# Optimization experiments

Measured on AMD Instinct MI355X. Metric: run time of the kernel, lower is better.

## Reference

```python
import jax, jax.numpy as jnp
import numpy as np

B, S, D = 4, 4096, 1024
GATE_THR = 0.0
ADAPT_RATIO = 0.25
MIN_K = 1
Q_MIX = 0.5
Q_WIN = 3
Q_THR = 0.5
Q_TEMP = 0.1
BUDGET_K = 2048  # ceil(0.5 * S)
CB_MIX = 0.3
CB_SIZE = 16
CB_TEMP = 0.1
CB_TOPK = 4


def setup_inputs() -> dict:
    key = jax.random.key(0)
    ks = jax.random.split(key, 6)
    x = jax.random.normal(ks[0], (B, S, D), dtype=jnp.float32)
    Wq = jax.random.normal(ks[1], (D, D), dtype=jnp.float32) * 0.02
    Wk = jax.random.normal(ks[2], (D, D), dtype=jnp.float32) * 0.02
    Wg = jax.random.normal(ks[3], (D, D), dtype=jnp.float32) * 0.02
    bg = jnp.zeros((D,), dtype=jnp.float32)
    Wm = jax.random.normal(ks[4], (D, D), dtype=jnp.float32) * 0.02
    bm = jnp.zeros((D,), dtype=jnp.float32)
    Wc = jax.random.normal(ks[5], (CB_SIZE, D), dtype=jnp.float32) * 0.02
    return {"x": x, "Wq": Wq, "Wk": Wk, "Wg": Wg, "bg": bg, "Wm": Wm, "bm": bm, "Wc": Wc}


def reference(x, Wq, Wk, Wg, bg, Wm, bm, Wc):
    # --- symplectic twist: cross-product area of consecutive (q, k) transitions ---
    q = x @ Wq.T                                 # [B,S,D]
    k = x @ Wk.T                                 # [B,S,D]
    twist = q[:, :-1] * k[:, 1:] - q[:, 1:] * k[:, :-1]   # [B,S-1,D]
    twist = jnp.pad(twist, ((0, 0), (1, 0), (0, 0)))       # pad first step -> [B,S,D]

    # --- gated SAE-style projection with adaptive top-k sparsity mask ---
    gate_pre = x @ Wg.T + bg                     # [B,S,D]
    strength = jnp.tanh(jnp.mean(jnp.abs(gate_pre), axis=-1, keepdims=True))
    kk = jnp.clip(jnp.ceil(strength * (ADAPT_RATIO * D)).astype(jnp.int32), MIN_K, D)  # [B,S,1]
    order = jnp.argsort(-gate_pre, axis=-1)      # descending rank order
    ranks = jnp.argsort(order, axis=-1)          # inverse permutation: rank of each feature
    topk_mask = ranks < kk                       # keep top-k features per token
    gate = ((gate_pre > GATE_THR) & topk_mask).astype(x.dtype)  # hard gate
    mag = jax.nn.relu(x @ Wm.T + bm)
    mu = gate * mag * twist                      # gated moment-map features [B,S,D]

    complexity = jnp.mean(jnp.abs(mu), axis=-1, keepdims=True)  # [B,S,1]

    # --- quorum consensus smoothing (avg_pool1d, count_include_pad) + budgeted top-k ---
    pad = Q_WIN // 2
    cpad = jnp.pad(complexity, ((0, 0), (pad, pad), (0, 0)))
    cs = jnp.pad(jnp.cumsum(cpad, axis=1), ((0, 0), (1, 0), (0, 0)))
    local = (cs[:, Q_WIN:] - cs[:, :-Q_WIN]) / Q_WIN            # [B,S,1] sliding mean
    quorum = jax.nn.sigmoid((local - Q_THR) / Q_TEMP)
    qr = quorum[..., 0]                                          # [B,S]
    top_idx = jax.lax.top_k(qr, BUDGET_K)[1]                     # [B,BUDGET_K]
    bmask = jnp.zeros_like(qr, dtype=bool).at[jnp.arange(B)[:, None], top_idx].set(True)
    quorum = jnp.where(bmask[..., None], quorum, 0.0)
    complexity = complexity * (1.0 - Q_MIX + Q_MIX * quorum)

    # --- codebook soft-assignment + top-k renorm + temporal shift score ---
    logits = (x @ Wc.T) / CB_TEMP                                # [B,S,CB_SIZE]
    probs = jax.nn.softmax(logits, axis=-1)
    ti = jax.lax.top_k(probs, CB_TOPK)[1]                        # [B,S,CB_TOPK]
    cmask = jnp.zeros(probs.shape, dtype=bool).at[
        jnp.arange(B)[:, None, None], jnp.arange(S)[None, :, None], ti].set(True)
    probs = jnp.where(cmask, probs, 0.0)
    probs = probs / jnp.clip(jnp.sum(probs, axis=-1, keepdims=True), 1e-8)
    shift = 0.5 * jnp.sum(jnp.abs(probs[:, 1:] - probs[:, :-1]), axis=-1, keepdims=True)
    cb_score = jnp.pad(shift, ((0, 0), (1, 0), (0, 0)))          # [B,S,1]

    complexity = (1.0 - CB_MIX) * complexity + CB_MIX * cb_score
    return complexity
```

## Files before the change

### kernel.cpp

```cpp
#include <hip/hip_runtime.h>
#include <hip/hip_bf16.h>
#include <cstdint>

#define BB 4
#define SS 4096
#define DD 1024
#define MM (BB * SS)
#define NTOT 4096
#define BUDGET 2048

typedef __attribute__((ext_vector_type(8))) short short8v;
typedef __attribute__((ext_vector_type(4))) float f32x4;

__device__ __forceinline__ float bf2f(unsigned int h) {
  return __uint_as_float(h << 16);
}
__device__ __forceinline__ unsigned short f2bf(float f) {
  unsigned int u = __float_as_uint(f);
  u = u + 0x7FFFu + ((u >> 16) & 1u);
  return (unsigned short)(u >> 16);
}
__device__ __forceinline__ unsigned int pkbf(float lo, float hi) {
  float2 f; f.x = lo; f.y = hi;
  __hip_bfloat162 h = __float22bfloat162_rn(f);
  return *(unsigned int*)&h;
}

__global__ __launch_bounds__(256) void convert2_kernel(
    const float* __restrict__ x,
    const float* __restrict__ Wq, const float* __restrict__ Wk,
    const float* __restrict__ Wg, const float* __restrict__ Wm,
    const float* __restrict__ Wc,
    unsigned short* __restrict__ xb, unsigned short* __restrict__ Wb,
    float* __restrict__ probs)
{
  const int blk = blockIdx.x;
  const int t = threadIdx.x;
  if (blk < 4096) {
    const int wv = t >> 6, ln = t & 63;
    const int token = blk * 4 + wv;
    const size_t rowo = (size_t)token * DD;
    const float4* x4 = (const float4*)(x + rowo);
    const float4* Wc4 = (const float4*)Wc;
    float4 xv[4];
    #pragma unroll
    for (int e = 0; e < 4; ++e) xv[e] = x4[e * 64 + ln];
    uint2* xo = (uint2*)(xb + rowo);
    #pragma unroll
    for (int e = 0; e < 4; ++e) {
      uint2 o; o.x = pkbf(xv[e].x, xv[e].y); o.y = pkbf(xv[e].z, xv[e].w);
      xo[e * 64 + ln] = o;
    }
    float pj[16];
    #pragma unroll
    for (int j = 0; j < 16; ++j) {
      float a = 0.f;
      #pragma unroll
      for (int e = 0; e < 4; ++e) {
        const float4 w = Wc4[j * 256 + e * 64 + ln];
        a += xv[e].x * w.x + xv[e].y * w.y + xv[e].z * w.z + xv[e].w * w.w;
      }
      pj[j] = a;
    }
    #pragma unroll
    for (int j = 0; j < 16; ++j) {
      #pragma unroll
      for (int off = 1; off < 64; off <<= 1) pj[j] += __shfl_xor(pj[j], off);
    }
    if (ln == 0) {
      float p[16];
      float mx = -3.4e38f;
      #pragma unroll
      for (int j = 0; j < 16; ++j) { p[j] = pj[j] * 10.0f; mx = fmaxf(mx, p[j]); }
      float se = 0.f;
      #pragma unroll
      for (int j = 0; j < 16; ++j) { p[j] = expf(p[j] - mx); se += p[j]; }
      const float inv = 1.0f / se;
      #pragma unroll
      for (int j = 0; j < 16; ++j) p[j] *= inv;
      unsigned int mk = 0;
      for (int it = 0; it < 4; ++it) {
        int bi = 0; float bv = -1.f;
        #pragma unroll
        for (int j = 0; j < 16; ++j)
          if (!((mk >> j) & 1u) && p[j] > bv) { bv = p[j]; bi = j; }
        mk |= 1u << bi;
      }
      float ssum = 0.f;
      #pragma unroll
      for (int j = 0; j < 16; ++j) if ((mk >> j) & 1u) ssum += p[j];
      const float rinv = 1.0f / fmaxf(ssum, 1e-8f);
      #pragma unroll
      for (int j = 0; j < 16; ++j)
        probs[(size_t)token * 16 + j] = ((mk >> j) & 1u) ? p[j] * rinv : 0.f;
    }
  } else {
    const size_t off0 = (size_t)(blk - 4096) * 2048 + t * 8;
    const int m = (int)(off0 >> 20);
    const float* Ws = (m == 0) ? Wq : (m == 1) ? Wk : (m == 2) ? Wg : Wm;
    const size_t wo = off0 & 1048575u;
    const float4 a0 = *(const float4*)(Ws + wo);
    const float4 a1 = *(const float4*)(Ws + wo + 4);
    uint4 o;
    o.x = pkbf(a0.x, a0.y); o.y = pkbf(a0.z, a0.w);
    o.z = pkbf(a1.x, a1.y); o.w = pkbf(a1.z, a1.w);
    *(uint4*)(Wb + off0) = o;
  }
}

__global__ __launch_bounds__(1024, 4) void gemm256_kernel(
    const unsigned short* __restrict__ xb, const unsigned short* __restrict__ Wb,
    const float* __restrict__ bg, const float* __restrict__ bm,
    unsigned short* __restrict__ qb, unsigned short* __restrict__ kb,
    unsigned short* __restrict__ gb, unsigned short* __restrict__ mb)
{
  __shared__ __align__(16) unsigned short lds[32768];
  const int t  = threadIdx.x;
  const int wv = t >> 6, ln = t & 63;
  const int wr = wv >> 2, wc = wv & 3;
  const int frow = ln & 15, kc = ln >> 4;

  const int o  = blockIdx.y * 16 + blockIdx.x;
  const int L  = (o & 7) * 128 + (o >> 3);
  const int bx = L & 15, by = L >> 4;
  const int m0 = by * 256;
  const int n0 = bx * 256;
  const int mat = n0 >> 10;
  const int nc0 = n0 & 1023;

  f32x4 acc[4][4];
  #pragma unroll
  for (int i = 0; i < 4; ++i)
    #pragma unroll
    for (int j = 0; j < 4; ++j) { acc[i][j][0]=0.f; acc[i][j][1]=0.f; acc[i][j][2]=0.f; acc[i][j][3]=0.f; }

  const int grow = t >> 2;
  const int gch  = (((t & 3) ^ ((t >> 2) & 3)) << 3);
  auto stage = [&](int buf, int kt) {
    const int k0 = kt << 5;
    const unsigned short* ga = xb + (size_t)(m0 + grow) * DD + k0 + gch;
    const unsigned short* gw = Wb + (size_t)(n0 + grow) * DD + k0 + gch;
    __builtin_amdgcn_global_load_lds(
        (const __attribute__((address_space(1))) void*)ga,
        (__attribute__((address_space(3))) void*)((__attribute__((address_space(3))) char*)lds
            + buf * 32768 + t * 16),
        16, 0, 0);
    __builtin_amdgcn_global_load_lds(
        (const __attribute__((address_space(1))) void*)gw,
        (__attribute__((address_space(3))) void*)((__attribute__((address_space(3))) char*)lds
            + buf * 32768 + 16384 + t * 16),
        16, 0, 0);
  };

  stage(0, 0);
  const int sl = ((kc ^ (frow & 3)) << 3);

  for (int kt = 0; kt < 32; ++kt) {
    const int cur = kt & 1;
    if (kt < 31) {
      stage(cur ^ 1, kt + 1);
      asm volatile("s_waitcnt vmcnt(2)" ::: "memory");
    } else {
      asm volatile("s_waitcnt vmcnt(0)" ::: "memory");
    }
    __builtin_amdgcn_s_barrier();
    asm volatile("" ::: "memory");

    short8v a[4], b[4];
    #pragma unroll
    for (int i = 0; i < 4; ++i)
      a[i] = *(const short8v*)&lds[cur * 16384 + (wr * 64 + i * 16 + frow) * 32 + sl];
    #pragma unroll
    for (int j = 0; j < 4; ++j)
      b[j] = *(const short8v*)&lds[cur * 16384 + 8192 + (wc * 64 + j * 16 + frow) * 32 + sl];

    #pragma unroll
    for (int i = 0; i < 4; ++i)
      #pragma unroll
      for (int j = 0; j < 4; ++j)
        acc[i][j] = __builtin_amdgcn_mfma_f32_16x16x32_bf16(a[i], b[j], acc[i][j], 0, 0, 0);

    asm volatile("" ::: "memory");
    __builtin_amdgcn_s_barrier();
  }

  unsigned short* outp = (mat == 0) ? qb : (mat == 1) ? kb : (mat == 2) ? gb : mb;
  #pragma unroll
  for (int i = 0; i < 4; ++i) {
    #pragma unroll
    for (int j = 0; j < 4; ++j) {
      const int col = nc0 + wc * 64 + j * 16 + frow;
      const float bias = (mat == 2) ? bg[col] : (mat == 3) ? bm[col] : 0.f;
      #pragma unroll
      for (int r = 0; r < 4; ++r) {
        const int row = m0 + wr * 64 + i * 16 + kc * 4 + r;
        float v = acc[i][j][r] + bias;
        if (mat == 3) v = fmaxf(v, 0.0f);
        outp[(size_t)row * DD + col] = f2bf(v);
      }
    }
  }
}

__global__ __launch_bounds__(256) void mfma_gemm_fb(
    const float* __restrict__ x,
    const float* __restrict__ Wq, const float* __restrict__ Wk,
    const float* __restrict__ Wg, const float* __restrict__ Wm,
    const float* __restrict__ bg, const float* __restrict__ bm,
    unsigned short* __restrict__ q_o, unsigned short* __restrict__ k_o,
    unsigned short* __restrict__ g_o, unsigned short* __restrict__ m_o)
{
  __shared__ __align__(16) unsigned short As[128 * 32];
  __shared__ __align__(16) unsigned short Bs[128 * 32];
  const int t  = threadIdx.x;
  const int wv = t >> 6, ln = t & 63;
  const int wr = wv >> 1, wc = wv & 1;
  const int m0 = blockIdx.y * 128;
  const int n0 = blockIdx.x * 128;
  const int mat = n0 >> 10;
  const int nc0 = n0 & 1023;
  const float* __restrict__ Wsrc = (mat == 0) ? Wq : (mat == 1) ? Wk : (mat == 2) ? Wg : Wm;

  f32x4 acc[4][4];
  #pragma unroll
  for (int i = 0; i < 4; ++i)
    #pragma unroll
    for (int j = 0; j < 4; ++j) { acc[i][j][0]=0.f; acc[i][j][1]=0.f; acc[i][j][2]=0.f; acc[i][j][3]=0.f; }

  const int frow = ln & 15, kc = ln >> 4;

  for (int k0 = 0; k0 < DD; k0 += 32) {
    #pragma unroll
    for (int c = 0; c < 2; ++c) {
      const int i = c * 256 + t;
      const int row = i >> 2, colc = i & 3;
      const float* ga = x    + (size_t)(m0 + row) * DD + k0 + (colc << 3);
      const float* gw = Wsrc + (size_t)(nc0 + row) * DD + k0 + (colc << 3);
      const float4 a0 = *(const float4*)ga, a1 = *(const float4*)(ga + 4);
      const float4 b0 = *(const float4*)gw, b1 = *(const float4*)(gw + 4);
      uint4 ao, bo;
      ao.x = pkbf(a0.x, a0.y); ao.y = pkbf(a0.z, a0.w);
      ao.z = pkbf(a1.x, a1.y); ao.w = pkbf(a1.z, a1.w);
      bo.x = pkbf(b0.x, b0.y); bo.y = pkbf(b0.z, b0.w);
      bo.z = pkbf(b1.x, b1.y); bo.w = pkbf(b1.z, b1.w);
      *(uint4*)&As[row * 32 + colc * 8] = ao;
      *(uint4*)&Bs[row * 32 + colc * 8] = bo;
    }
    __syncthreads();
    short8v a[4], b[4];
    #pragma unroll
    for (int i = 0; i < 4; ++i) {
      a[i] = *(const short8v*)&As[(wr * 64 + i * 16 + frow) * 32 + kc * 8];
      b[i] = *(const short8v*)&Bs[(wc * 64 + i * 16 + frow) * 32 + kc * 8];
    }
    #pragma unroll
    for (int i = 0; i < 4; ++i)
      #pragma unroll
      for (int j = 0; j < 4; ++j)
        acc[i][j] = __builtin_amdgcn_mfma_f32_16x16x32_bf16(a[i], b[j], acc[i][j], 0, 0, 0);
    __syncthreads();
  }

  unsigned short* outp = (mat == 0) ? q_o : (mat == 1) ? k_o : (mat == 2) ? g_o : m_o;
  #pragma unroll
  for (int i = 0; i < 4; ++i) {
    #pragma unroll
    for (int j = 0; j < 4; ++j) {
      const int col = nc0 + wc * 64 + j * 16 + frow;
      #pragma unroll
      for (int r = 0; r < 4; ++r) {
        const int row = m0 + wr * 64 + i * 16 + kc * 4 + r;
        float v = acc[i][j][r];
        if (mat == 2) v += bg[col];
        if (mat == 3) v = fmaxf(v + bm[col], 0.0f);
        outp[(size_t)row * DD + col] = f2bf(v);
      }
    }
  }
}

__global__ __launch_bounds__(256) void token_kernel3(
    const unsigned short* __restrict__ qb, const unsigned short* __restrict__ kb,
    const unsigned short* __restrict__ gb, const unsigned short* __restrict__ mb,
    float* __restrict__ craw)
{
  const int wv = threadIdx.x >> 6;
  const int ln = threadIdx.x & 63;
  const int token = blockIdx.x * 4 + wv;
  const int s = token & (SS - 1);
  const size_t rowo = (size_t)token * DD;

  if (s == 0) { if (ln == 0) craw[token] = 0.f; return; }

  unsigned short gbit[16];
  *(uint4*)&gbit[0] = *(const uint4*)(gb + rowo + ln * 16);
  *(uint4*)&gbit[8] = *(const uint4*)(gb + rowo + ln * 16 + 8);
  int ckey[16];
  float asum = 0.f;
  #pragma unroll
  for (int i = 0; i < 16; ++i) {
    const unsigned int b = gbit[i];
    ckey[i] = (b & 0x8000u) ? (int)(b ^ 0xFFFFu) : (int)(b | 0x8000u);
    asum += bf2f(b & 0x7FFFu);
  }
  #pragma unroll
  for (int off = 1; off < 64; off <<= 1) asum += __shfl_xor(asum, off);
  const float strength = tanhf(asum * (1.0f / 1024.0f));
  int kkv = (int)ceilf(strength * 256.0f);
  kkv = min(max(kkv, 1), 1024);

  int lo = 0, hi = 0xFFFF;
  while (lo < hi) {
    const int mid = (lo + hi + 1) >> 1;
    int c = 0;
    #pragma unroll
    for (int i = 0; i < 16; ++i) c += (ckey[i] >= mid);
    #pragma unroll
    for (int off = 1; off < 64; off <<= 1) c += __shfl_xor(c, off);
    if (c >= kkv) lo = mid; else hi = mid - 1;
  }
  const int T = lo;

  int cg = 0, myeq = 0;
  #pragma unroll
  for (int i = 0; i < 16; ++i) { cg += (ckey[i] > T); myeq += (ckey[i] == T); }
  #pragma unroll
  for (int off = 1; off < 64; off <<= 1) cg += __shfl_xor(cg, off);
  int incl = myeq;
  #pragma unroll
  for (int off = 1; off < 64; off <<= 1) {
    const int tt = __shfl_up(incl, off);
    if (ln >= off) incl += tt;
  }
  int ebase = incl - myeq;
  const int keep_eq = kkv - cg;

  unsigned short mB[16], qcB[16], kcB[16], qpB[16], kpB[16];
  *(uint4*)&mB[0]  = *(const uint4*)(mb + rowo + ln * 16);
  *(uint4*)&mB[8]  = *(const uint4*)(mb + rowo + ln * 16 + 8);
  *(uint4*)&qcB[0] = *(const uint4*)(qb + rowo + ln * 16);
  *(uint4*)&qcB[8] = *(const uint4*)(qb + rowo + ln * 16 + 8);
  *(uint4*)&kcB[0] = *(const uint4*)(kb + rowo + ln * 16);
  *(uint4*)&kcB[8] = *(const uint4*)(kb + rowo + ln * 16 + 8);
  *(uint4*)&qpB[0] = *(const uint4*)(qb + rowo - DD + ln * 16);
  *(uint4*)&qpB[8] = *(const uint4*)(qb + rowo - DD + ln * 16 + 8);
  *(uint4*)&kpB[0] = *(const uint4*)(kb + rowo - DD + ln * 16);
  *(uint4*)&kpB[8] = *(const uint4*)(kb + rowo - DD + ln * 16 + 8);

  float accv = 0.f;
  #pragma unroll
  for (int i = 0; i < 16; ++i) {
    const bool kp_ = (ckey[i] > T) || (ckey[i] == T && ebase < keep_eq);
    if (ckey[i] == T) ebase++;
    const unsigned int b = gbit[i];
    const bool gpos = (!(b & 0x8000u)) && (b != 0u);
    if (gpos && kp_) {
      const float tw = bf2f(qpB[i]) * bf2f(kcB[i]) - bf2f(qcB[i]) * bf2f(kpB[i]);
      accv += bf2f(mB[i]) * fabsf(tw);
    }
  }
  #pragma unroll
  for (int off = 1; off < 64; off <<= 1) accv += __shfl_xor(accv, off);
  if (ln == 0) craw[token] = accv * (1.0f / 1024.0f);
}

__global__ __launch_bounds__(256) void token_kernel2(
    const float* __restrict__ x, const float* __restrict__ Wc,
    const unsigned short* __restrict__ qb, const unsigned short* __restrict__ kb,
    const unsigned short* __restrict__ gb, const unsigned short* __restrict__ mb,
    float* __restrict__ probs, float* __restrict__ craw)
{
  const int wv = threadIdx.x >> 6;
  const int ln = threadIdx.x & 63;
  const int token = blockIdx.x * 4 + wv;
  const int s = token & (SS - 1);
  const size_t rowo = (size_t)token * DD;

  const float4* x4 = (const float4*)(x + rowo);
  const float4* Wc4 = (const float4*)Wc;
  float4 xv[4];
  #pragma unroll
  for (int e = 0; e < 4; ++e) xv[e] = x4[e * 64 + ln];
  float pj[16];
  #pragma unroll
  for (int j = 0; j < 16; ++j) {
    float a = 0.f;
    #pragma unroll
    for (int e = 0; e < 4; ++e) {
      const float4 w = Wc4[j * 256 + e * 64 + ln];
      a += xv[e].x * w.x + xv[e].y * w.y + xv[e].z * w.z + xv[e].w * w.w;
    }
    pj[j] = a;
  }
  #pragma unroll
  for (int j = 0; j < 16; ++j) {
    #pragma unroll
    for (int off = 1; off < 64; off <<= 1) pj[j] += __shfl_xor(pj[j], off);
  }
  if (ln == 0) {
    float p[16];
    float mx = -3.4e38f;
    #pragma unroll
    for (int j = 0; j < 16; ++j) { p[j] = pj[j] * 10.0f; mx = fmaxf(mx, p[j]); }
    float se = 0.f;
    #pragma unroll
    for (int j = 0; j < 16; ++j) { p[j] = expf(p[j] - mx); se += p[j]; }
    const float inv = 1.0f / se;
    #pragma unroll
    for (int j = 0; j < 16; ++j) p[j] *= inv;
    unsigned int mk = 0;
    for (int it = 0; it < 4; ++it) {
      int bi = 0; float bv = -1.f;
      #pragma unroll
      for (int j = 0; j < 16; ++j)
        if (!((mk >> j) & 1u) && p[j] > bv) { bv = p[j]; bi = j; }
      mk |= 1u << bi;
    }
    float ssum = 0.f;
    #pragma unroll
    for (int j = 0; j < 16; ++j) if ((mk >> j) & 1u) ssum += p[j];
    const float rinv = 1.0f / fmaxf(ssum, 1e-8f);
    #pragma unroll
    for (int j = 0; j < 16; ++j)
      probs[(size_t)token * 16 + j] = ((mk >> j) & 1u) ? p[j] * rinv : 0.f;
  }

  if (s == 0) { if (ln == 0) craw[token] = 0.f; return; }

  unsigned short gbit[16];
  *(uint4*)&gbit[0] = *(const uint4*)(gb + rowo + ln * 16);
  *(uint4*)&gbit[8] = *(const uint4*)(gb + rowo + ln * 16 + 8);
  int ckey[16];
  float asum = 0.f;
  #pragma unroll
  for (int i = 0; i < 16; ++i) {
    const unsigned int b = gbit[i];
    ckey[i] = (b & 0x8000u) ? (int)(b ^ 0xFFFFu) : (int)(b | 0x8000u);
    asum += bf2f(b & 0x7FFFu);
  }
  #pragma unroll
  for (int off = 1; off < 64; off <<= 1) asum += __shfl_xor(asum, off);
  const float strength = tanhf(asum * (1.0f / 1024.0f));
  int kkv = (int)ceilf(strength * 256.0f);
  kkv = min(max(kkv, 1), 1024);

  int lo = 0, hi = 0xFFFF;
  while (lo < hi) {
    const int mid = (lo + hi + 1) >> 1;
    int c = 0;
    #pragma unroll
    for (int i = 0; i < 16; ++i) c += (ckey[i] >= mid);
    #pragma unroll
    for (int off = 1; off < 64; off <<= 1) c += __shfl_xor(c, off);
    if (c >= kkv) lo = mid; else hi = mid - 1;
  }
  const int T = lo;

  int cg = 0, myeq = 0;
  #pragma unroll
  for (int i = 0; i < 16; ++i) { cg += (ckey[i] > T); myeq += (ckey[i] == T); }
  #pragma unroll
  for (int off = 1; off < 64; off <<= 1) cg += __shfl_xor(cg, off);
  int incl = myeq;
  #pragma unroll
  for (int off = 1; off < 64; off <<= 1) {
    const int tt = __shfl_up(incl, off);
    if (ln >= off) incl += tt;
  }
  int ebase = incl - myeq;
  const int keep_eq = kkv - cg;

  unsigned short mB[16], qcB[16], kcB[16], qpB[16], kpB[16];
  *(uint4*)&mB[0]  = *(const uint4*)(mb + rowo + ln * 16);
  *(uint4*)&mB[8]  = *(const uint4*)(mb + rowo + ln * 16 + 8);
  *(uint4*)&qcB[0] = *(const uint4*)(qb + rowo + ln * 16);
  *(uint4*)&qcB[8] = *(const uint4*)(qb + rowo + ln * 16 + 8);
  *(uint4*)&kcB[0] = *(const uint4*)(kb + rowo + ln * 16);
  *(uint4*)&kcB[8] = *(const uint4*)(kb + rowo + ln * 16 + 8);
  *(uint4*)&qpB[0] = *(const uint4*)(qb + rowo - DD + ln * 16);
  *(uint4*)&qpB[8] = *(const uint4*)(qb + rowo - DD + ln * 16 + 8);
  *(uint4*)&kpB[0] = *(const uint4*)(kb + rowo - DD + ln * 16);
  *(uint4*)&kpB[8] = *(const uint4*)(kb + rowo - DD + ln * 16 + 8);

  float accv = 0.f;
  #pragma unroll
  for (int i = 0; i < 16; ++i) {
    const bool kp_ = (ckey[i] > T) || (ckey[i] == T && ebase < keep_eq);
    if (ckey[i] == T) ebase++;
    const unsigned int b = gbit[i];
    const bool gpos = (!(b & 0x8000u)) && (b != 0u);
    if (gpos && kp_) {
      const float tw = bf2f(qpB[i]) * bf2f(kcB[i]) - bf2f(qcB[i]) * bf2f(kpB[i]);
      accv += bf2f(mB[i]) * fabsf(tw);
    }
  }
  #pragma unroll
  for (int off = 1; off < 64; off <<= 1) accv += __shfl_xor(accv, off);
  if (ln == 0) craw[token] = accv * (1.0f / 1024.0f);
}

__global__ __launch_bounds__(256) void quorum_kernel(
    const float* __restrict__ craw, const float* __restrict__ probs,
    float* __restrict__ quorum, float* __restrict__ cb)
{
  const int idx = blockIdx.x * 256 + threadIdx.x;
  const int s = idx & (SS - 1);
  const float c1 = craw[idx];
  const float c0 = (s > 0) ? craw[idx - 1] : 0.f;
  const float c2 = (s < SS - 1) ? craw[idx + 1] : 0.f;
  const float local = (c0 + c1 + c2) / 3.0f;
  quorum[idx] = 1.0f / (1.0f + expf((0.5f - local) * 10.0f));
  float sh = 0.f;
  if (s > 0) {
    #pragma unroll
    for (int j = 0; j < 16; ++j)
      sh += fabsf(probs[(size_t)idx * 16 + j] - probs[(size_t)(idx - 1) * 16 + j]);
  }
  cb[idx] = 0.5f * sh;
}

__global__ __launch_bounds__(64) void final_kernel(
    const float* __restrict__ craw, const float* __restrict__ quorum,
    const float* __restrict__ cb, float* __restrict__ outp)
{
  const int b = blockIdx.x;
  const int ln = threadIdx.x;
  const size_t base = (size_t)b * SS;
  float qv[64]; unsigned int key[64];
  #pragma unroll
  for (int i = 0; i < 64; ++i) {
    qv[i] = quorum[base + ln * 64 + i];
    const unsigned int bb = __float_as_uint(qv[i]);
    key[i] = (bb & 0x80000000u) ? ~bb : (bb | 0x80000000u);
  }
  unsigned int lo = 0u, hi = 0xFFFFFFFFu;
  while (lo < hi) {
    const unsigned int mid = (unsigned int)(((unsigned long long)lo + hi + 1ull) >> 1);
    int c = 0;
    #pragma unroll
    for (int i = 0; i < 64; ++i) c += (key[i] >= mid);
    #pragma unroll
    for (int off = 1; off < 64; off <<= 1) c += __shfl_xor(c, off);
    if (c >= BUDGET) lo = mid; else hi = mid - 1;
  }
  const unsigned int T = lo;
  int cg = 0, myeq = 0;
  #pragma unroll
  for (int i = 0; i < 64; ++i) { cg += (key[i] > T); myeq += (key[i] == T); }
  #pragma unroll
  for (int off = 1; off < 64; off <<= 1) cg += __shfl_xor(cg, off);
  int scan = myeq;
  #pragma unroll
  for (int off = 1; off < 64; off <<= 1) {
    const int nsc = __shfl_up(scan, off);
    if (ln >= off) scan += nsc;
  }
  int ebase = scan - myeq;
  const int keep_eq = BUDGET - cg;
  #pragma unroll
  for (int i = 0; i < 64; ++i) {
    const size_t sidx = base + (size_t)ln * 64 + i;
    const bool kp_ = (key[i] > T) || (key[i] == T && ebase < keep_eq);
    if (key[i] == T) ebase++;
    const float q = kp_ ? qv[i] : 0.f;
    outp[sidx] = 0.7f * (craw[sidx] * (0.5f + 0.5f * q)) + 0.3f * cb[sidx];
  }
}

extern "C" void kernel_launch(void* const* d_in, const int* in_sizes, int n_in,
                              void* d_out, int out_size, void* d_ws, size_t ws_size,
                              hipStream_t stream)
{
  const float* x  = (const float*)d_in[0];
  const float* Wq = (const float*)d_in[1];
  const float* Wk = (const float*)d_in[2];
  const float* Wg = (const float*)d_in[3];
  const float* bg = (const float*)d_in[4];
  const float* Wm = (const float*)d_in[5];
  const float* bm = (const float*)d_in[6];
  const float* Wc = (const float*)d_in[7];
  float* outp = (float*)d_out;
  char* w = (char*)d_ws;

  const size_t SZ_BF = (size_t)MM * DD * 2;
  const size_t SMALL_OFF = 4 * SZ_BF;
  const size_t SZ_SMALL = 1048576 + 3 * 65536;

  unsigned short* qb = (unsigned short*)(w);
  unsigned short* kb = (unsigned short*)(w + SZ_BF);
  unsigned short* gb = (unsigned short*)(w + 2 * SZ_BF);
  unsigned short* mb = (unsigned short*)(w + 3 * SZ_BF);
  char* sm = w + SMALL_OFF;
  float* probs  = (float*)(sm);
  float* craw   = (float*)(sm + 1048576);
  float* quorum = (float*)(sm + 1048576 + 65536);
  float* cbuf   = (float*)(sm + 1048576 + 2 * 65536);

  const size_t need_mid = SMALL_OFF + SZ_SMALL + SZ_BF + (size_t)4 * 1048576 * 2;

  if (ws_size >= need_mid) {
    unsigned short* xb = (unsigned short*)(sm + SZ_SMALL);
    unsigned short* Wb = xb + (size_t)MM * DD;
    convert2_kernel<<<dim3(4096 + 2048), 256, 0, stream>>>(
        x, Wq, Wk, Wg, Wm, Wc, xb, Wb, probs);
    gemm256_kernel<<<dim3(NTOT / 256, MM / 256), 1024, 0, stream>>>(
        xb, Wb, bg, bm, qb, kb, gb, mb);
    token_kernel3<<<dim3(MM / 4), 256, 0, stream>>>(qb, kb, gb, mb, craw);
  } else {
    mfma_gemm_fb<<<dim3(NTOT / 128, MM / 128), 256, 0, stream>>>(
        x, Wq, Wk, Wg, Wm, bg, bm, qb, kb, gb, mb);
    token_kernel2<<<dim3(MM / 4), 256, 0, stream>>>(x, Wc, qb, kb, gb, mb, probs, craw);
  }
  quorum_kernel<<<dim3(MM / 256), 256, 0, stream>>>(craw, probs, quorum, cbuf);
  final_kernel<<<dim3(BB), 64, 0, stream>>>(craw, quorum, cbuf, outp);
}
```

Baseline: 277.9 us.

## Load GEMM B operand directly to registers and fuse quorum and final tail kernels

```diff
diff --git a/kernel.cpp b/kernel.cpp
--- a/kernel.cpp
+++ b/kernel.cpp
@@ -114,7 +114,7 @@
     unsigned short* __restrict__ qb, unsigned short* __restrict__ kb,
     unsigned short* __restrict__ gb, unsigned short* __restrict__ mb)
 {
-  __shared__ __align__(16) unsigned short lds[32768];
+  __shared__ __align__(16) unsigned short lds[16384];
   const int t  = threadIdx.x;
   const int wv = t >> 6, ln = t & 63;
   const int wr = wv >> 2, wc = wv & 3;
@@ -134,54 +134,62 @@
     #pragma unroll
     for (int j = 0; j < 4; ++j) { acc[i][j][0]=0.f; acc[i][j][1]=0.f; acc[i][j][2]=0.f; acc[i][j][3]=0.f; }
 
-  const int grow = t >> 2;
-  const int gch  = (((t & 3) ^ ((t >> 2) & 3)) << 3);
-  auto stage = [&](int buf, int kt) {
-    const int k0 = kt << 5;
-    const unsigned short* ga = xb + (size_t)(m0 + grow) * DD + k0 + gch;
-    const unsigned short* gw = Wb + (size_t)(n0 + grow) * DD + k0 + gch;
+  const int arow = t >> 2;
+  const int ach  = (t & 3) << 3;
+  auto stageA = [&](int buf, int kt) {
+    const unsigned short* ga = xb + (size_t)(m0 + arow) * DD + (kt << 5) + ach;
     __builtin_amdgcn_global_load_lds(
         (const __attribute__((address_space(1))) void*)ga,
         (__attribute__((address_space(3))) void*)((__attribute__((address_space(3))) char*)lds
-            + buf * 32768 + t * 16),
-        16, 0, 0);
-    __builtin_amdgcn_global_load_lds(
-        (const __attribute__((address_space(1))) void*)gw,
-        (__attribute__((address_space(3))) void*)((__attribute__((address_space(3))) char*)lds
-            + buf * 32768 + 16384 + t * 16),
+            + buf * 16384 + t * 16),
         16, 0, 0);
   };
 
-  stage(0, 0);
-  const int sl = ((kc ^ (frow & 3)) << 3);
-
-  for (int kt = 0; kt < 32; ++kt) {
-    const int cur = kt & 1;
-    if (kt < 31) {
-      stage(cur ^ 1, kt + 1);
-      asm volatile("s_waitcnt vmcnt(2)" ::: "memory");
-    } else {
-      asm volatile("s_waitcnt vmcnt(0)" ::: "memory");
-    }
-    __builtin_amdgcn_s_barrier();
-    asm volatile("" ::: "memory");
-
-    short8v a[4], b[4];
-    #pragma unroll
-    for (int i = 0; i < 4; ++i)
-      a[i] = *(const short8v*)&lds[cur * 16384 + (wr * 64 + i * 16 + frow) * 32 + sl];
+  const unsigned short* wb0 = Wb + (size_t)(n0 + wc * 64 + frow) * DD + (kc << 3);
+  auto loadBv = [&](short8v bd[4], int kt) {
+    const int k0 = kt << 5;
     #pragma unroll
     for (int j = 0; j < 4; ++j)
-      b[j] = *(const short8v*)&lds[cur * 16384 + 8192 + (wc * 64 + j * 16 + frow) * 32 + sl];
-
-    #pragma unroll
-    for (int i = 0; i < 4; ++i)
-      #pragma unroll
-      for (int j = 0; j < 4; ++j)
-        acc[i][j] = __builtin_amdgcn_mfma_f32_16x16x32_bf16(a[i], b[j], acc[i][j], 0, 0, 0);
-
-    asm volatile("" ::: "memory");
-    __builtin_amdgcn_s_barrier();
+      bd[j] = *(const short8v*)(wb0 + (size_t)(j * 16) * DD + k0);
+  };
+
+  short8v b0[4], b1[4];
+  stageA(0, 0);
+  loadBv(b0, 0);
+  __syncthreads();
+
+  for (int kt2 = 0; kt2 < 16; ++kt2) {
+    const int e = kt2 * 2;
+    stageA(1, e + 1);
+    loadBv(b1, e + 1);
+    {
+      short8v a[4];
+      #pragma unroll
+      for (int i = 0; i < 4; ++i)
+        a[i] = *(const short8v*)&lds[(wr * 64 + i * 16 + frow) * 32 + (kc << 3)];
+      #pragma unroll
+      for (int i = 0; i < 4; ++i)
+        #pragma unroll
+        for (int j = 0; j < 4; ++j)
+          acc[i][j] = __builtin_amdgcn_mfma_f32_16x16x32_bf16(a[i], b0[j], acc[i][j], 0, 0, 0);
+    }
+    __syncthreads();
+    if (kt2 < 15) {
+      stageA(0, e + 2);
+      loadBv(b0, e + 2);
+    }
+    {
+      short8v a[4];
+      #pragma unroll
+      for (int i = 0; i < 4; ++i)
+        a[i] = *(const short8v*)&lds[8192 + (wr * 64 + i * 16 + frow) * 32 + (kc << 3)];
+      #pragma unroll
+      for (int i = 0; i < 4; ++i)
+        #pragma unroll
+        for (int j = 0; j < 4; ++j)
+          acc[i][j] = __builtin_amdgcn_mfma_f32_16x16x32_bf16(a[i], b1[j], acc[i][j], 0, 0, 0);
+    }
+    __syncthreads();
   }
 
   unsigned short* outp = (mat == 0) ? qb : (mat == 1) ? kb : (mat == 2) ? gb : mb;
@@ -499,71 +507,76 @@
   if (ln == 0) craw[token] = accv * (1.0f / 1024.0f);
 }
 
-__global__ __launch_bounds__(256) void quorum_kernel(
+__global__ __launch_bounds__(256) void tail_kernel(
     const float* __restrict__ craw, const float* __restrict__ probs,
-    float* __restrict__ quorum, float* __restrict__ cb)
+    float* __restrict__ outp)
 {
-  const int idx = blockIdx.x * 256 + threadIdx.x;
-  const int s = idx & (SS - 1);
-  const float c1 = craw[idx];
-  const float c0 = (s > 0) ? craw[idx - 1] : 0.f;
-  const float c2 = (s < SS - 1) ? craw[idx + 1] : 0.f;
-  const float local = (c0 + c1 + c2) / 3.0f;
-  quorum[idx] = 1.0f / (1.0f + expf((0.5f - local) * 10.0f));
-  float sh = 0.f;
-  if (s > 0) {
-    #pragma unroll
-    for (int j = 0; j < 16; ++j)
-      sh += fabsf(probs[(size_t)idx * 16 + j] - probs[(size_t)(idx - 1) * 16 + j]);
-  }
-  cb[idx] = 0.5f * sh;
-}
-
-__global__ __launch_bounds__(64) void final_kernel(
-    const float* __restrict__ craw, const float* __restrict__ quorum,
-    const float* __restrict__ cb, float* __restrict__ outp)
-{
+  __shared__ float qs[SS];
+  __shared__ float cs_[SS];
   const int b = blockIdx.x;
-  const int ln = threadIdx.x;
+  const int t = threadIdx.x;
   const size_t base = (size_t)b * SS;
-  float qv[64]; unsigned int key[64];
-  #pragma unroll
-  for (int i = 0; i < 64; ++i) {
-    qv[i] = quorum[base + ln * 64 + i];
-    const unsigned int bb = __float_as_uint(qv[i]);
-    key[i] = (bb & 0x80000000u) ? ~bb : (bb | 0x80000000u);
-  }
-  unsigned int lo = 0u, hi = 0xFFFFFFFFu;
-  while (lo < hi) {
-    const unsigned int mid = (unsigned int)(((unsigned long long)lo + hi + 1ull) >> 1);
-    int c = 0;
-    #pragma unroll
-    for (int i = 0; i < 64; ++i) c += (key[i] >= mid);
-    #pragma unroll
-    for (int off = 1; off < 64; off <<= 1) c += __shfl_xor(c, off);
-    if (c >= BUDGET) lo = mid; else hi = mid - 1;
-  }
-  const unsigned int T = lo;
-  int cg = 0, myeq = 0;
-  #pragma unroll
-  for (int i = 0; i < 64; ++i) { cg += (key[i] > T); myeq += (key[i] == T); }
-  #pragma unroll
-  for (int off = 1; off < 64; off <<= 1) cg += __shfl_xor(cg, off);
-  int scan = myeq;
-  #pragma unroll
-  for (int off = 1; off < 64; off <<= 1) {
-    const int nsc = __shfl_up(scan, off);
-    if (ln >= off) scan += nsc;
-  }
-  int ebase = scan - myeq;
-  const int keep_eq = BUDGET - cg;
-  #pragma unroll
-  for (int i = 0; i < 64; ++i) {
-    const size_t sidx = base + (size_t)ln * 64 + i;
-    const bool kp_ = (key[i] > T) || (key[i] == T && ebase < keep_eq);
-    if (key[i] == T) ebase++;
-    const float q = kp_ ? qv[i] : 0.f;
-    outp[sidx] = 0.7f * (craw[sidx] * (0.5f + 0.5f * q)) + 0.3f * cb[sidx];
+
+  #pragma unroll
+  for (int i = 0; i < 16; ++i) {
+    const int s = t * 16 + i;
+    const float c1 = craw[base + s];
+    const float c0 = (s > 0) ? craw[base + s - 1] : 0.f;
+    const float c2 = (s < SS - 1) ? craw[base + s + 1] : 0.f;
+    const float local = (c0 + c1 + c2) / 3.0f;
+    qs[s] = 1.0f / (1.0f + expf((0.5f - local) * 10.0f));
+    float sh = 0.f;
+    if (s > 0) {
+      #pragma unroll
+      for (int j = 0; j < 16; ++j)
+        sh += fabsf(probs[(base + s) * 16 + j] - probs[(base + s - 1) * 16 + j]);
+    }
+    cs_[s] = 0.5f * sh;
+  }
+  __syncthreads();
+
+  if (t < 64) {
+    const int ln = t;
+    float qv[64]; unsigned int key[64];
+    #pragma unroll
+    for (int i = 0; i < 64; ++i) {
+      qv[i] = qs[ln * 64 + i];
+      const unsigned int bb = __float_as_uint(qv[i]);
+      key[i] = (bb & 0x80000000u) ? ~bb : (bb | 0x80000000u);
+    }
+    unsigned int lo = 0u, hi = 0xFFFFFFFFu;
+    while (lo < hi) {
+      const unsigned int mid = (unsigned int)(((unsigned long long)lo + hi + 1ull) >> 1);
+      int c = 0;
+      #pragma unroll
+      for (int i = 0; i < 64; ++i) c += (key[i] >= mid);
+      #pragma unroll
+      for (int off = 1; off < 64; off <<= 1) c += __shfl_xor(c, off);
+      if (c >= BUDGET) lo = mid; else hi = mid - 1;
+    }
+    const unsigned int T = lo;
+    int cg = 0, myeq = 0;
+    #pragma unroll
+    for (int i = 0; i < 64; ++i) { cg += (key[i] > T); myeq += (key[i] == T); }
+    #pragma unroll
+    for (int off = 1; off < 64; off <<= 1) cg += __shfl_xor(cg, off);
+    int scan = myeq;
+    #pragma unroll
+    for (int off = 1; off < 64; off <<= 1) {
+      const int nsc = __shfl_up(scan, off);
+      if (ln >= off) scan += nsc;
+    }
+    int ebase = scan - myeq;
+    const int keep_eq = BUDGET - cg;
+    #pragma unroll
+    for (int i = 0; i < 64; ++i) {
+      const int s = ln * 64 + i;
+      const size_t sidx = base + s;
+      const bool kp_ = (key[i] > T) || (key[i] == T && ebase < keep_eq);
+      if (key[i] == T) ebase++;
+      const float q = kp_ ? qv[i] : 0.f;
+      outp[sidx] = 0.7f * (craw[sidx] * (0.5f + 0.5f * q)) + 0.3f * cs_[s];
+    }
   }
 }
 
@@ -584,7 +597,7 @@
 
   const size_t SZ_BF = (size_t)MM * DD * 2;
   const size_t SMALL_OFF = 4 * SZ_BF;
-  const size_t SZ_SMALL = 1048576 + 3 * 65536;
+  const size_t SZ_SMALL = 1048576 + 65536;
 
   unsigned short* qb = (unsigned short*)(w);
   unsigned short* kb = (unsigned short*)(w + SZ_BF);
@@ -593,8 +606,6 @@
   char* sm = w + SMALL_OFF;
   float* probs  = (float*)(sm);
   float* craw   = (float*)(sm + 1048576);
-  float* quorum = (float*)(sm + 1048576 + 65536);
-  float* cbuf   = (float*)(sm + 1048576 + 2 * 65536);
 
   const size_t need_mid = SMALL_OFF + SZ_SMALL + SZ_BF + (size_t)4 * 1048576 * 2;
 
@@ -611,6 +622,5 @@
         x, Wq, Wk, Wg, Wm, bg, bm, qb, kb, gb, mb);
     token_kernel2<<<dim3(MM / 4), 256, 0, stream>>>(x, Wc, qb, kb, gb, mb, probs, craw);
   }
-  quorum_kernel<<<dim3(MM / 256), 256, 0, stream>>>(craw, probs, quorum, cbuf);
-  final_kernel<<<dim3(BB), 64, 0, stream>>>(craw, quorum, cbuf, outp);
-}
+  tail_kernel<<<dim3(BB), 256, 0, stream>>>(craw, probs, outp);
+}
```

Result: slower. 454.6 us (+63.6%).
